# Performance work log

Measured on AMD Instinct MI355X. Metric: run time of the kernel, lower is better.

The kernel has to match this reference:

```python
import jax, jax.numpy as jnp
import numpy as np

H = 256; NH = 4; DH = H // NH
NT, NS, NV = 4096, 2048, 1024
E1, E2, E3 = 65536, 16384, 32768
LN_EPS = 1e-5


def setup_inputs() -> dict:
    key = jax.random.key(0)
    ks = jax.random.split(key, 40)
    def nrm(i, shape):
        return jax.random.normal(ks[i], shape, jnp.float32) * 0.05
    inp = {
        "x_term": jax.random.normal(ks[0], (NT, H), jnp.float32),
        "x_symbol": jax.random.normal(ks[1], (NS, H), jnp.float32),
        "x_var": jax.random.normal(ks[2], (NV, H), jnp.float32),
        "ha_src": jax.random.randint(ks[3], (E1,), 0, NT),
        "ha_dst": jax.random.randint(ks[4], (E1,), 0, NT),
        "so_src": jax.random.randint(ks[5], (E2,), 0, NT),
        "so_dst": jax.random.randint(ks[6], (E2,), 0, NS),
        "vo_src": jax.random.randint(ks[7], (E3,), 0, NV),
        "vo_dst": jax.random.randint(ks[8], (E3,), 0, NT),
        # SAGEConv params for the 4 term-destination relations
        "Wl_rha": nrm(9, (H, H)),  "bl_rha": nrm(10, (H,)), "Wr_rha": nrm(11, (H, H)),
        "Wl_ha":  nrm(12, (H, H)), "bl_ha":  nrm(13, (H,)), "Wr_ha":  nrm(14, (H, H)),
        "Wl_rsym": nrm(15, (H, H)), "bl_rsym": nrm(16, (H,)), "Wr_rsym": nrm(17, (H, H)),
        "Wl_var": nrm(18, (H, H)), "bl_var": nrm(19, (H,)), "Wr_var": nrm(20, (H, H)),
        "ln_g": jnp.ones((H,), jnp.float32),
        "ln_b": jnp.zeros((H,), jnp.float32),
        "in_proj_w": nrm(21, (3 * H, H)),
        "in_proj_b": nrm(22, (3 * H,)),
        "out_proj_w": nrm(23, (H, H)),
        "out_proj_b": nrm(24, (H,)),
        "post_w": nrm(25, (H, H)),
        "post_b": nrm(26, (H,)),
    }
    return inp


def _sage(x_src, x_dst, src, dst, Wl, bl, Wr, num_dst):
    # PyG SAGEConv: lin_l(mean_j x_src[j]) + lin_r(x_dst)
    msg = x_src[src]                                            # [E, H] gather
    s = jax.ops.segment_sum(msg, dst, num_segments=num_dst)     # [N_dst, H] scatter-add
    cnt = jax.ops.segment_sum(jnp.ones((src.shape[0],), x_src.dtype), dst,
                              num_segments=num_dst)
    agg = s / jnp.maximum(cnt, 1.0)[:, None]
    return agg @ Wl.T + bl + x_dst @ Wr.T


def _layernorm(x, g, b):
    mu = jnp.mean(x, axis=-1, keepdims=True)
    var = jnp.mean(jnp.square(x - mu), axis=-1, keepdims=True)
    return (x - mu) * jax.lax.rsqrt(var + LN_EPS) * g + b


def _mha(x, in_w, in_b, out_w, out_b):
    # torch MultiheadAttention (eval, batch=1, self-attention)
    qkv = x @ in_w.T + in_b                       # [N, 3H]
    q, k, v = jnp.split(qkv, 3, axis=-1)
    def heads(t):
        return t.reshape(-1, NH, DH).transpose(1, 0, 2)  # [NH, N, DH]
    q, k, v = heads(q), heads(k), heads(v)
    scores = jnp.einsum("hqd,hkd->hqk", q, k) / np.sqrt(DH).astype(np.float32)
    a = jax.nn.softmax(scores, axis=-1)
    o = jnp.einsum("hqk,hkd->hqd", a, v)          # [NH, N, DH]
    o = o.transpose(1, 0, 2).reshape(-1, H)
    return o @ out_w.T + out_b


def reference(x_term, x_symbol, x_var,
              ha_src, ha_dst, so_src, so_dst, vo_src, vo_dst,
              Wl_rha, bl_rha, Wr_rha, Wl_ha, bl_ha, Wr_ha,
              Wl_rsym, bl_rsym, Wr_rsym, Wl_var, bl_var, Wr_var,
              ln_g, ln_b, in_proj_w, in_proj_b, out_proj_w, out_proj_b,
              post_w, post_b):
    nt = x_term.shape[0]
    # HeteroConv(aggr='sum') over the 4 relations whose destination is 'term'
    conv_term = (
        _sage(x_term, x_term, ha_dst, ha_src, Wl_rha, bl_rha, Wr_rha, nt)    # rev_has_arg
        + _sage(x_term, x_term, ha_src, ha_dst, Wl_ha, bl_ha, Wr_ha, nt)     # has_arg
        + _sage(x_symbol, x_term, so_dst, so_src, Wl_rsym, bl_rsym, Wr_rsym, nt)  # rev_symbol_of
        + _sage(x_var, x_term, vo_src, vo_dst, Wl_var, bl_var, Wr_var, nt)   # var_occurrence
    )
    term_out = _layernorm(conv_term + x_term, ln_g, ln_b)  # dropout is identity in eval
    attn_out = _mha(term_out, in_proj_w, in_proj_b, out_proj_w, out_proj_b)
    post = jax.nn.relu(attn_out @ post_w.T + post_b)
    term_final = post + term_out
    return term_final
```

## Files before the change

kernel.cpp:

```cpp
#include <hip/hip_runtime.h>
#include <hip/hip_bf16.h>

#define H 256
#define NT 4096
#define NHEAD 4
#define E1 65536
#define E2 16384
#define E3 32768
#define TOTE (2 * E1 + E2 + E3)
#define LN_EPS 1e-5f
#define SPLIT 4

typedef __hip_bfloat16 bf16;
typedef short bf16x8 __attribute__((ext_vector_type(8)));
typedef float f32x4 __attribute__((ext_vector_type(4)));

__device__ __forceinline__ float b2f(bf16 v) { return __bfloat162float(v); }
__device__ __forceinline__ float u2f(unsigned short u) {
    unsigned int x = ((unsigned int)u) << 16;
    return __uint_as_float(x);
}
__device__ __forceinline__ unsigned short f2u(float f) {
    bf16 h = __float2bfloat16(f);
    unsigned short v;
    __builtin_memcpy(&v, &h, 2);
    return v;
}
__device__ __forceinline__ unsigned short f2u_rtz(float f) {
    return (unsigned short)(__float_as_uint(f) >> 16);
}
__device__ __forceinline__ float ldin(const void* p, size_t i, bool isbf) {
    return isbf ? b2f(((const bf16*)p)[i]) : ((const float*)p)[i];
}

__global__ __launch_bounds__(256) void k_init(float4* cnt4, int n4,
                                              const unsigned int* __restrict__ lng,
                                              unsigned int* __restrict__ flag) {
    int i = blockIdx.x * 256 + threadIdx.x;
    if (i == 0) *flag = (lng[0] == 0x3F803F80u) ? 1u : 0u;
    int stride = gridDim.x * 256;
    float4 z = make_float4(0.f, 0.f, 0.f, 0.f);
    for (; i < n4; i += stride) cnt4[i] = z;
}

__global__ __launch_bounds__(256) void k_count4(const int* __restrict__ s0, const int* __restrict__ s1,
                                                const int* __restrict__ s2, const int* __restrict__ s3,
                                                int* __restrict__ cnt) {
    int i = blockIdx.x * 256 + threadIdx.x;
    int r, e;
    if (i < E1) { r = 0; e = i; }
    else if (i < 2 * E1) { r = 1; e = i - E1; }
    else if (i < 2 * E1 + E2) { r = 2; e = i - 2 * E1; }
    else if (i < TOTE) { r = 3; e = i - 2 * E1 - E2; }
    else return;
    const int* s = (r == 0) ? s0 : (r == 1) ? s1 : (r == 2) ? s2 : s3;
    atomicAdd(&cnt[r * NT + s[e]], 1);
}

__global__ __launch_bounds__(256) void k_scan(const int* __restrict__ cnt, int* __restrict__ offs,
                                              int* __restrict__ cursor) {
    __shared__ int tot[256];
    int t = threadIdx.x, r = blockIdx.x;
    const int* c = cnt + r * NT;
    int* o = offs + r * (NT + 1);
    int* cur = cursor + r * NT;
    int base = t * 16;
    int local[16];
    int sum = 0;
#pragma unroll
    for (int j = 0; j < 16; j++) { local[j] = c[base + j]; sum += local[j]; }
    tot[t] = sum;
    __syncthreads();
    if (t == 0) {
        int run = 0;
        for (int i = 0; i < 256; i++) { int v = tot[i]; tot[i] = run; run += v; }
        o[NT] = run;
    }
    __syncthreads();
    int run = tot[t];
#pragma unroll
    for (int j = 0; j < 16; j++) { o[base + j] = run; cur[base + j] = run; run += local[j]; }
}

__global__ __launch_bounds__(256) void k_fill(const int* __restrict__ s0, const int* __restrict__ s1,
                                              const int* __restrict__ s2, const int* __restrict__ s3,
                                              const int* __restrict__ g0, const int* __restrict__ g1,
                                              const int* __restrict__ g2, const int* __restrict__ g3,
                                              int* __restrict__ cursor, int* __restrict__ csr) {
    int i = blockIdx.x * 256 + threadIdx.x;
    int r, e, rb;
    if (i < E1) { r = 0; e = i; rb = 0; }
    else if (i < 2 * E1) { r = 1; e = i - E1; rb = E1; }
    else if (i < 2 * E1 + E2) { r = 2; e = i - 2 * E1; rb = 2 * E1; }
    else if (i < TOTE) { r = 3; e = i - 2 * E1 - E2; rb = 2 * E1 + E2; }
    else return;
    const int* s = (r == 0) ? s0 : (r == 1) ? s1 : (r == 2) ? s2 : s3;
    const int* g = (r == 0) ? g0 : (r == 1) ? g1 : (r == 2) ? g2 : g3;
    int d = s[e];
    int pos = atomicAdd(&cursor[r * NT + d], 1);
    csr[rb + pos] = g[e];
}

__global__ __launch_bounds__(256) void k_gatherA(
    const void* __restrict__ x0, const void* __restrict__ x1,
    const void* __restrict__ x2, const void* __restrict__ x3,
    const int* __restrict__ offs, const int* __restrict__ csr,
    bf16* __restrict__ aggs, const unsigned int* __restrict__ flag) {
    int y = blockIdx.y;
    int i = blockIdx.x * 4 + (threadIdx.x >> 6);
    int lane = threadIdx.x & 63;
    bool isbf = (*flag != 0u);
    const void* x = (y == 0) ? x0 : (y == 1) ? x1 : (y == 2) ? x2 : x3;
    static const int rbase[4] = {0, E1, 2 * E1, 2 * E1 + E2};
    const int* o = offs + y * (NT + 1);
    const int* cs = csr + rbase[y];
    int b = o[i], e = o[i + 1];
    float ax = 0.f, ay = 0.f, az = 0.f, aw = 0.f;
    if (isbf) {
        for (int j = b; j < e; j++) {
            int s = cs[j];
            ushort4 u = *(const ushort4*)((const unsigned short*)x + (size_t)s * H + lane * 4);
            ax += u2f(u.x); ay += u2f(u.y); az += u2f(u.z); aw += u2f(u.w);
        }
    } else {
        for (int j = b; j < e; j++) {
            int s = cs[j];
            float4 v = *(const float4*)((const float*)x + (size_t)s * H + lane * 4);
            ax += v.x; ay += v.y; az += v.z; aw += v.w;
        }
    }
    float inv = 1.0f / fmaxf((float)(e - b), 1.0f);
    *(ushort4*)((unsigned short*)aggs + ((size_t)y * NT + i) * H + lane * 4) =
        make_ushort4(f2u(ax * inv), f2u(ay * inv), f2u(az * inv), f2u(aw * inv));
}

__global__ __launch_bounds__(256) void k_prepB(
    const void* __restrict__ Wl0, const void* __restrict__ Wl1,
    const void* __restrict__ Wl2, const void* __restrict__ Wl3,
    const void* __restrict__ Wr0, const void* __restrict__ Wr1,
    const void* __restrict__ Wr2, const void* __restrict__ Wr3,
    const void* __restrict__ b0, const void* __restrict__ b1,
    const void* __restrict__ b2, const void* __restrict__ b3,
    bf16* __restrict__ Bcat, float* __restrict__ bsum, const unsigned int* __restrict__ flag) {
    int idx = blockIdx.x * 256 + threadIdx.x;
    bool isbf = (*flag != 0u);
    int n = idx / 1280, k = idx % 1280;
    float v;
    if (k < 1024) {
        const void* W = (k < 256) ? Wl0 : (k < 512) ? Wl1 : (k < 768) ? Wl2 : Wl3;
        v = ldin(W, (size_t)n * 256 + (k & 255), isbf);
    } else {
        size_t o = (size_t)n * 256 + (k - 1024);
        v = ldin(Wr0, o, isbf) + ldin(Wr1, o, isbf) + ldin(Wr2, o, isbf) + ldin(Wr3, o, isbf);
    }
    ((unsigned short*)Bcat)[idx] = f2u(v);
    if (idx < 256)
        bsum[idx] = ldin(b0, idx, isbf) + ldin(b1, idx, isbf) + ldin(b2, idx, isbf) + ldin(b3, idx, isbf);
}

__global__ __launch_bounds__(256) void k_convln(
    const bf16* __restrict__ aggs, const bf16* __restrict__ Bcat, const float* __restrict__ bsum,
    const void* __restrict__ xt, const void* __restrict__ gw, const void* __restrict__ gb,
    bf16* __restrict__ term, const unsigned int* __restrict__ flag) {
    __shared__ unsigned short Asm[8 * 16 * 8];
    __shared__ unsigned short Bsm[8 * 256 * 8];
    __shared__ float redS[4][16];
    const bool isbf = (*flag != 0u);
    const int tid = threadIdx.x;
    const int w = tid >> 6, lane = tid & 63;
    const int col = lane & 15, quad = lane >> 4;
    const int m0 = blockIdx.x * 16;
    const int srow = tid & 63, skq = tid >> 6;

    f32x4 acc[4];
#pragma unroll
    for (int dt = 0; dt < 4; dt++) acc[dt] = (f32x4){0.f, 0.f, 0.f, 0.f};

    bf16x8 areg;
    bf16x8 breg[8];
    auto loadA = [&](int k0) {
        if (tid < 128) {
            int row = tid & 15, akq = tid >> 4;
            int k = k0 + akq * 8;
            if (k < 1024) {
                areg = *(const bf16x8*)((const unsigned short*)aggs +
                                        ((size_t)(k >> 8) * NT + m0 + row) * 256 + (k & 255));
            } else {
#pragma unroll
                for (int j = 0; j < 8; j++)
                    areg[j] = (short)f2u(ldin(xt, (size_t)(m0 + row) * 256 + (k - 1024) + j, isbf));
            }
        }
    };
    auto loadB = [&](int k0) {
#pragma unroll
        for (int t = 0; t < 4; t++)
#pragma unroll
            for (int kk = 0; kk < 2; kk++)
                breg[t * 2 + kk] = *(const bf16x8*)((const unsigned short*)Bcat +
                                       (size_t)(t * 64 + srow) * 1280 + k0 + (skq * 2 + kk) * 8);
    };

    loadA(0);
    loadB(0);
    for (int k0 = 0; k0 < 1280; k0 += 64) {
        __syncthreads();
        if (tid < 128) *(bf16x8*)&Asm[tid * 8] = areg;
#pragma unroll
        for (int t = 0; t < 4; t++)
#pragma unroll
            for (int kk = 0; kk < 2; kk++)
                *(bf16x8*)&Bsm[((skq * 2 + kk) * 256 + t * 64 + srow) * 8] = breg[t * 2 + kk];
        __syncthreads();
        if (k0 + 64 < 1280) { loadA(k0 + 64); loadB(k0 + 64); }
#pragma unroll
        for (int ch = 0; ch < 2; ch++) {
            bf16x8 a = *(const bf16x8*)&Asm[(((ch * 4 + quad) & 7) * 16 + col) * 8];
#pragma unroll
            for (int dt = 0; dt < 4; dt++) {
                bf16x8 b = *(const bf16x8*)&Bsm[((ch * 4 + quad) * 256 + w * 64 + dt * 16 + col) * 8];
                acc[dt] = __builtin_amdgcn_mfma_f32_16x16x32_bf16(a, b, acc[dt], 0, 0, 0);
            }
        }
    }

#pragma unroll
    for (int dt = 0; dt < 4; dt++) {
        int n = w * 64 + dt * 16 + col;
        float bsv = bsum[n];
#pragma unroll
        for (int r = 0; r < 4; r++) {
            int m = m0 + quad * 4 + r;
            acc[dt][r] += bsv + ldin(xt, (size_t)m * 256 + n, isbf);
        }
    }
    float mu[4], rs_[4];
#pragma unroll
    for (int r = 0; r < 4; r++) {
        float s = acc[0][r] + acc[1][r] + acc[2][r] + acc[3][r];
#pragma unroll
        for (int mk = 1; mk <= 8; mk <<= 1) s += __shfl_xor(s, mk);
        if (col == 0) redS[w][quad * 4 + r] = s;
    }
    __syncthreads();
#pragma unroll
    for (int r = 0; r < 4; r++) {
        int m = quad * 4 + r;
        mu[r] = (redS[0][m] + redS[1][m] + redS[2][m] + redS[3][m]) * (1.0f / 256.0f);
    }
    __syncthreads();
#pragma unroll
    for (int r = 0; r < 4; r++) {
        float s2 = 0.f;
#pragma unroll
        for (int dt = 0; dt < 4; dt++) {
            float d = acc[dt][r] - mu[r];
            s2 += d * d;
        }
#pragma unroll
        for (int mk = 1; mk <= 8; mk <<= 1) s2 += __shfl_xor(s2, mk);
        if (col == 0) redS[w][quad * 4 + r] = s2;
    }
    __syncthreads();
#pragma unroll
    for (int r = 0; r < 4; r++) {
        int m = quad * 4 + r;
        float var = (redS[0][m] + redS[1][m] + redS[2][m] + redS[3][m]) * (1.0f / 256.0f);
        rs_[r] = rsqrtf(var + LN_EPS);
    }
#pragma unroll
    for (int dt = 0; dt < 4; dt++) {
        int n = w * 64 + dt * 16 + col;
        float gv = ldin(gw, n, isbf), bv = ldin(gb, n, isbf);
#pragma unroll
        for (int r = 0; r < 4; r++) {
            int m = m0 + quad * 4 + r;
            term[(size_t)m * 256 + n] = __float2bfloat16((acc[dt][r] - mu[r]) * rs_[r] * gv + bv);
        }
    }
}

template <int AMODE, int EPI>
__global__ __launch_bounds__(256) void k_gemm(
    const void* __restrict__ A, const void* __restrict__ A2, const float* __restrict__ ml,
    const void* __restrict__ B, const void* __restrict__ bias,
    const bf16* __restrict__ resid, bf16* __restrict__ vt, void* __restrict__ outp,
    int M, int N, int K, const unsigned int* __restrict__ flag) {
    __shared__ unsigned short Asm[8 * 64 * 8];
    __shared__ unsigned short Bsm[8 * 64 * 8];
    const bool isbf = (*flag != 0u);
    const int tid = threadIdx.x;
    const int w = tid >> 6, lane = tid & 63;
    const int col = lane & 15, quad = lane >> 4;
    const int m0 = blockIdx.x * 64, n0 = blockIdx.y * 64;
    const int srow = tid & 63, skq = tid >> 6;
    const int am = m0 + srow;

    f32x4 acc[4];
#pragma unroll
    for (int dt = 0; dt < 4; dt++) acc[dt] = (f32x4){0.f, 0.f, 0.f, 0.f};

    bf16x8 areg[2], breg[2];
    auto loadA = [&](int k0) {
#pragma unroll
        for (int c = 0; c < 2; c++) {
            int k = k0 + skq * 16 + c * 8;
            if (AMODE == 0) {
                areg[c] = *(const bf16x8*)((const unsigned short*)A + (size_t)am * K + k);
            } else {
                int h = k >> 6;
                float l0 = ml[(size_t)(0 * NHEAD + h) * NT + am];
                float l1 = ml[(size_t)(1 * NHEAD + h) * NT + am];
                float l2 = ml[(size_t)(2 * NHEAD + h) * NT + am];
                float l3 = ml[(size_t)(3 * NHEAD + h) * NT + am];
                float iw = 1.0f / (l0 + l1 + l2 + l3);
                bf16x8 o0 = *(const bf16x8*)((const unsigned short*)A + (size_t)am * H + k);
                bf16x8 o1 = *(const bf16x8*)((const unsigned short*)A + ((size_t)NT + am) * H + k);
                bf16x8 o2 = *(const bf16x8*)((const unsigned short*)A2 + (size_t)am * H + k);
                bf16x8 o3 = *(const bf16x8*)((const unsigned short*)A2 + ((size_t)NT + am) * H + k);
#pragma unroll
                for (int j = 0; j < 8; j++)
                    areg[c][j] = (short)f2u((l0 * u2f((unsigned short)o0[j]) + l1 * u2f((unsigned short)o1[j]) +
                                             l2 * u2f((unsigned short)o2[j]) + l3 * u2f((unsigned short)o3[j])) * iw);
            }
        }
    };
    auto loadB = [&](int k0) {
#pragma unroll
        for (int c = 0; c < 2; c++) {
            size_t bi = (size_t)(n0 + srow) * K + k0 + skq * 16 + c * 8;
            if (isbf) {
                breg[c] = *(const bf16x8*)((const unsigned short*)B + bi);
            } else {
#pragma unroll
                for (int j = 0; j < 8; j++) breg[c][j] = (short)f2u(((const float*)B)[bi + j]);
            }
        }
    };

    loadA(0);
    loadB(0);
    for (int k0 = 0; k0 < K; k0 += 64) {
        __syncthreads();
#pragma unroll
        for (int c = 0; c < 2; c++) {
            *(bf16x8*)&Asm[((skq * 2 + c) * 64 + srow) * 8] = areg[c];
            *(bf16x8*)&Bsm[((skq * 2 + c) * 64 + srow) * 8] = breg[c];
        }
        __syncthreads();
        if (k0 + 64 < K) { loadA(k0 + 64); loadB(k0 + 64); }
#pragma unroll
        for (int ch = 0; ch < 2; ch++) {
            bf16x8 a = *(const bf16x8*)&Asm[((ch * 4 + quad) * 64 + w * 16 + col) * 8];
#pragma unroll
            for (int dt = 0; dt < 4; dt++) {
                bf16x8 b = *(const bf16x8*)&Bsm[((ch * 4 + quad) * 64 + dt * 16 + col) * 8];
                acc[dt] = __builtin_amdgcn_mfma_f32_16x16x32_bf16(a, b, acc[dt], 0, 0, 0);
            }
        }
    }
#pragma unroll
    for (int dt = 0; dt < 4; dt++) {
        int n = n0 + dt * 16 + col;
        float bv = ldin(bias, n, isbf);
        if (EPI == 3 && n0 >= 512) {
            int m = m0 + w * 16 + quad * 4;
            *(ushort4*)((unsigned short*)vt + (size_t)(n - 512) * NT + m) =
                make_ushort4(f2u(acc[dt][0] + bv), f2u(acc[dt][1] + bv),
                             f2u(acc[dt][2] + bv), f2u(acc[dt][3] + bv));
            continue;
        }
#pragma unroll
        for (int r = 0; r < 4; r++) {
            int m = m0 + w * 16 + quad * 4 + r;
            float v = acc[dt][r] + bv;
            if (EPI == 3) {
                ((bf16*)outp)[(size_t)m * 512 + n] = __float2bfloat16(v);
            } else if (EPI == 2) {
                size_t off = (size_t)m * N + n;
                v = fmaxf(v, 0.f);
                v += b2f(resid[off]);
                ((float*)outp)[off] = v;
            } else {
                ((bf16*)outp)[(size_t)m * N + n] = __float2bfloat16(v);
            }
        }
    }
}

__global__ __launch_bounds__(256) void k_attn(const bf16* __restrict__ qkvQK,
                                              const bf16* __restrict__ vt,
                                              bf16* __restrict__ opart01,
                                              bf16* __restrict__ opart23,
                                              float* __restrict__ ml) {
    __shared__ unsigned short Ksm[8 * 64 * 8];
    __shared__ unsigned short Vsm[8 * 64 * 8];
    __shared__ unsigned short Psm[4][2048];
    const int h = blockIdx.y, sp = blockIdx.z;
    const int q0 = blockIdx.x * 128;
    const int tid = threadIdx.x;
    const int w = tid >> 6, lane = tid & 63;
    const int col = lane & 15, quad = lane >> 4;
    const unsigned short* qk = (const unsigned short*)qkvQK;
    const unsigned short* vp = (const unsigned short*)vt;

    bf16x8 aQ[2][2];
#pragma unroll
    for (int qt = 0; qt < 2; qt++)
#pragma unroll
        for (int ch = 0; ch < 2; ch++)
            aQ[qt][ch] = *(const bf16x8*)(qk + (size_t)(q0 + qt * 64 + w * 16 + col) * 512 +
                                          h * 64 + ch * 32 + quad * 8);

    f32x4 O[2][4];
#pragma unroll
    for (int qt = 0; qt < 2; qt++)
#pragma unroll
        for (int dt = 0; dt < 4; dt++) O[qt][dt] = (f32x4){0.f, 0.f, 0.f, 0.f};
    float lsum[2] = {0.f, 0.f};

    const int kbeg = sp * (NT / SPLIT), kend = kbeg + NT / SPLIT;
    const float SC = 0.125f * 1.44269504f;
    const int pbase = col * 8 + (quad & 1) * 4 + (quad >> 1) * 128;

    bf16x8 kreg[2], vreg[2];
    auto loadKV = [&](int kb) {
#pragma unroll
        for (int it = 0; it < 2; it++) {
            int cid = tid + it * 256;
            int kkey = cid & 63, dhq = cid >> 6;
            kreg[it] = *(const bf16x8*)(qk + (size_t)(kb + kkey) * 512 + 256 + h * 64 + dhq * 8);
            int vd = cid & 63, vo = cid >> 6;
            vreg[it] = *(const bf16x8*)(vp + (size_t)(h * 64 + vd) * NT + kb + vo * 8);
        }
    };
    loadKV(kbeg);

    for (int kb = kbeg; kb < kend; kb += 64) {
        __syncthreads();
#pragma unroll
        for (int it = 0; it < 2; it++) {
            int cid = tid + it * 256;
            *(bf16x8*)&Ksm[cid * 8] = kreg[it];
            *(bf16x8*)&Vsm[cid * 8] = vreg[it];
        }
        __syncthreads();
        if (kb + 64 < kend) loadKV(kb + 64);

        f32x4 c0[4], c1[4];
#pragma unroll
        for (int dt = 0; dt < 4; dt++) {
            c0[dt] = (f32x4){0.f, 0.f, 0.f, 0.f};
            c1[dt] = (f32x4){0.f, 0.f, 0.f, 0.f};
#pragma unroll
            for (int ch = 0; ch < 2; ch++) {
                bf16x8 kf = *(const bf16x8*)&Ksm[((ch * 4 + quad) * 64 + dt * 16 + col) * 8];
                c0[dt] = __builtin_amdgcn_mfma_f32_16x16x32_bf16(kf, aQ[0][ch], c0[dt], 0, 0, 0);
                c1[dt] = __builtin_amdgcn_mfma_f32_16x16x32_bf16(kf, aQ[1][ch], c1[dt], 0, 0, 0);
            }
        }
#pragma unroll
        for (int qt = 0; qt < 2; qt++) {
#pragma unroll
            for (int dt = 0; dt < 4; dt++) {
                f32x4 cc = qt ? c1[dt] : c0[dt];
                float p0 = exp2f(cc[0] * SC), p1 = exp2f(cc[1] * SC);
                float p2 = exp2f(cc[2] * SC), p3 = exp2f(cc[3] * SC);
                lsum[qt] += (p0 + p1) + (p2 + p3);
                *(ushort4*)&Psm[w][qt * 1024 + dt * 256 + pbase] =
                    make_ushort4(f2u_rtz(p0), f2u_rtz(p1), f2u_rtz(p2), f2u_rtz(p3));
            }
        }
        bf16x8 aP[2][2];
#pragma unroll
        for (int qt = 0; qt < 2; qt++)
#pragma unroll
            for (int kc = 0; kc < 2; kc++)
                aP[qt][kc] = *(const bf16x8*)&Psm[w][qt * 1024 + (kc * 4 + quad) * 128 + col * 8];
#pragma unroll
        for (int dt = 0; dt < 4; dt++)
#pragma unroll
            for (int kc = 0; kc < 2; kc++) {
                bf16x8 b = *(const bf16x8*)&Vsm[((kc * 4 + quad) * 64 + dt * 16 + col) * 8];
                O[0][dt] = __builtin_amdgcn_mfma_f32_16x16x32_bf16(aP[0][kc], b, O[0][dt], 0, 0, 0);
                O[1][dt] = __builtin_amdgcn_mfma_f32_16x16x32_bf16(aP[1][kc], b, O[1][dt], 0, 0, 0);
            }
    }
#pragma unroll
    for (int qt = 0; qt < 2; qt++) {
        float l = lsum[qt];
        l += __shfl_xor(l, 16);
        l += __shfl_xor(l, 32);
        bf16* ob = (sp < 2) ? (opart01 + (size_t)sp * NT * H) : (opart23 + (size_t)(sp - 2) * NT * H);
        if (quad == 0)
            ml[((size_t)sp * NHEAD + h) * NT + (q0 + qt * 64 + w * 16 + col)] = l;
        float lr[4];
#pragma unroll
        for (int r = 0; r < 4; r++) lr[r] = __shfl(l, quad * 4 + r, 16);
#pragma unroll
        for (int dt = 0; dt < 4; dt++) {
#pragma unroll
            for (int r = 0; r < 4; r++) {
                int q = q0 + qt * 64 + w * 16 + quad * 4 + r;
                ob[(size_t)q * H + h * 64 + dt * 16 + col] = __float2bfloat16(O[qt][dt][r] / lr[r]);
            }
        }
    }
}

extern "C" void kernel_launch(void* const* d_in, const int* in_sizes, int n_in,
                              void* d_out, int out_size, void* d_ws, size_t ws_size,
                              hipStream_t stream) {
    const void* x_term   = d_in[0];
    const void* x_symbol = d_in[1];
    const void* x_var    = d_in[2];
    const int* ha_src = (const int*)d_in[3];
    const int* ha_dst = (const int*)d_in[4];
    const int* so_src = (const int*)d_in[5];
    const int* so_dst = (const int*)d_in[6];
    const int* vo_src = (const int*)d_in[7];
    const int* vo_dst = (const int*)d_in[8];
    const void* Wl[4]  = {d_in[9],  d_in[12], d_in[15], d_in[18]};
    const void* blv[4] = {d_in[10], d_in[13], d_in[16], d_in[19]};
    const void* Wr[4]  = {d_in[11], d_in[14], d_in[17], d_in[20]};
    const void* ln_g = d_in[21];
    const void* ln_b = d_in[22];
    const void* in_w = d_in[23];
    const void* in_b = d_in[24];
    const void* out_w = d_in[25];
    const void* out_b = d_in[26];
    const void* post_w = d_in[27];
    const void* post_b = d_in[28];

    char* ws = (char*)d_ws;
    unsigned int* flag = (unsigned int*)ws;
    char* csrbase = ws + 256;
    int* cnt    = (int*)csrbase;
    int* offs   = (int*)(csrbase + 65536);
    int* cursor = (int*)(csrbase + 132096);
    int* csr    = (int*)(csrbase + 197632);
    bf16*  Bcat = (bf16*)csrbase;
    float* bsum = (float*)(csrbase + 655360);
    float* ml   = (float*)csrbase;
    bf16* aggs  = (bf16*)(ws + (1 << 20));
    bf16* term  = (bf16*)(ws + (1 << 20) + 8388608);
    bf16* opart23 = (bf16*)(ws + (1 << 20) + 10485760);
    bf16* qkvQK = aggs;
    bf16* vt    = (bf16*)((char*)aggs + 4194304);
    bf16* proj  = aggs;
    bf16* opart01 = (bf16*)d_out;

    k_init<<<16, 256, 0, stream>>>((float4*)cnt, 4 * NT / 4, (const unsigned int*)ln_g, flag);
    k_count4<<<(TOTE + 255) / 256, 256, 0, stream>>>(ha_src, ha_dst, so_src, vo_dst, cnt);
    k_scan<<<4, 256, 0, stream>>>(cnt, offs, cursor);
    k_fill<<<(TOTE + 255) / 256, 256, 0, stream>>>(ha_src, ha_dst, so_src, vo_dst,
                                                   ha_dst, ha_src, so_dst, vo_src, cursor, csr);
    k_gatherA<<<dim3(NT / 4, 4), 256, 0, stream>>>(x_term, x_term, x_symbol, x_var,
                                                   offs, csr, aggs, flag);
    k_prepB<<<(256 * 1280) / 256, 256, 0, stream>>>(Wl[0], Wl[1], Wl[2], Wl[3],
                                                    Wr[0], Wr[1], Wr[2], Wr[3],
                                                    blv[0], blv[1], blv[2], blv[3],
                                                    Bcat, bsum, flag);

    k_convln<<<256, 256, 0, stream>>>(aggs, Bcat, bsum, x_term, ln_g, ln_b, term, flag);

    k_gemm<0, 3><<<dim3(64, 12), 256, 0, stream>>>(
        term, nullptr, nullptr, in_w, in_b, nullptr, vt, qkvQK, NT, 768, 256, flag);

    k_attn<<<dim3(32, NHEAD, SPLIT), 256, 0, stream>>>(qkvQK, vt, opart01, opart23, ml);

    k_gemm<1, 0><<<dim3(64, 4), 256, 0, stream>>>(
        opart01, opart23, ml, out_w, out_b, nullptr, nullptr, proj, NT, 256, 256, flag);

    k_gemm<0, 2><<<dim3(64, 4), 256, 0, stream>>>(
        proj, nullptr, nullptr, post_w, post_b, term, nullptr, d_out, NT, 256, 256, flag);

    (void)in_sizes; (void)n_in; (void)out_size; (void)ws_size;
}
```

Baseline: 276.9 us.

## Halve attention query tile to 64 rows, doubling blocks; add MFMA priority hints

The attention kernel now processes 64 queries per block instead of 128, doubling the grid to 1024 blocks and halving per-thread accumulator registers and the P buffer in LDS. This is meant to raise occupancy and parallelism on the many CUs. In exchange, each K/V tile loaded into shared memory is reused across half as many queries, doubling K/V global traffic. It also wraps the MFMA loops in s_setprio and switches to the hardware exp2 builtin.

```diff
diff --git a/kernel.cpp b/kernel.cpp
--- a/kernel.cpp
+++ b/kernel.cpp
@@ -395,29 +395,25 @@
                                               float* __restrict__ ml) {
     __shared__ unsigned short Ksm[8 * 64 * 8];
     __shared__ unsigned short Vsm[8 * 64 * 8];
-    __shared__ unsigned short Psm[4][2048];
+    __shared__ unsigned short Psm[4][1024];
     const int h = blockIdx.y, sp = blockIdx.z;
-    const int q0 = blockIdx.x * 128;
+    const int q0 = blockIdx.x * 64;
     const int tid = threadIdx.x;
     const int w = tid >> 6, lane = tid & 63;
     const int col = lane & 15, quad = lane >> 4;
     const unsigned short* qk = (const unsigned short*)qkvQK;
     const unsigned short* vp = (const unsigned short*)vt;
 
-    bf16x8 aQ[2][2];
-#pragma unroll
-    for (int qt = 0; qt < 2; qt++)
-#pragma unroll
-        for (int ch = 0; ch < 2; ch++)
-            aQ[qt][ch] = *(const bf16x8*)(qk + (size_t)(q0 + qt * 64 + w * 16 + col) * 512 +
-                                          h * 64 + ch * 32 + quad * 8);
-
-    f32x4 O[2][4];
-#pragma unroll
-    for (int qt = 0; qt < 2; qt++)
-#pragma unroll
-        for (int dt = 0; dt < 4; dt++) O[qt][dt] = (f32x4){0.f, 0.f, 0.f, 0.f};
-    float lsum[2] = {0.f, 0.f};
+    bf16x8 aQ[2];
+#pragma unroll
+    for (int ch = 0; ch < 2; ch++)
+        aQ[ch] = *(const bf16x8*)(qk + (size_t)(q0 + w * 16 + col) * 512 +
+                                  h * 64 + ch * 32 + quad * 8);
+
+    f32x4 O[4];
+#pragma unroll
+    for (int dt = 0; dt < 4; dt++) O[dt] = (f32x4){0.f, 0.f, 0.f, 0.f};
+    float lsum = 0.f;
 
     const int kbeg = sp * (NT / SPLIT), kend = kbeg + NT / SPLIT;
     const float SC = 0.125f * 1.44269504f;
@@ -447,63 +443,57 @@
         __syncthreads();
         if (kb + 64 < kend) loadKV(kb + 64);
 
-        f32x4 c0[4], c1[4];
+        f32x4 c[4];
+        __builtin_amdgcn_s_setprio(1);
 #pragma unroll
         for (int dt = 0; dt < 4; dt++) {
-            c0[dt] = (f32x4){0.f, 0.f, 0.f, 0.f};
-            c1[dt] = (f32x4){0.f, 0.f, 0.f, 0.f};
+            c[dt] = (f32x4){0.f, 0.f, 0.f, 0.f};
 #pragma unroll
             for (int ch = 0; ch < 2; ch++) {
                 bf16x8 kf = *(const bf16x8*)&Ksm[((ch * 4 + quad) * 64 + dt * 16 + col) * 8];
-                c0[dt] = __builtin_amdgcn_mfma_f32_16x16x32_bf16(kf, aQ[0][ch], c0[dt], 0, 0, 0);
-                c1[dt] = __builtin_amdgcn_mfma_f32_16x16x32_bf16(kf, aQ[1][ch], c1[dt], 0, 0, 0);
-            }
-        }
-#pragma unroll
-        for (int qt = 0; qt < 2; qt++) {
-#pragma unroll
-            for (int dt = 0; dt < 4; dt++) {
-                f32x4 cc = qt ? c1[dt] : c0[dt];
-                float p0 = exp2f(cc[0] * SC), p1 = exp2f(cc[1] * SC);
-                float p2 = exp2f(cc[2] * SC), p3 = exp2f(cc[3] * SC);
-                lsum[qt] += (p0 + p1) + (p2 + p3);
-                *(ushort4*)&Psm[w][qt * 1024 + dt * 256 + pbase] =
-                    make_ushort4(f2u_rtz(p0), f2u_rtz(p1), f2u_rtz(p2), f2u_rtz(p3));
-            }
-        }
-        bf16x8 aP[2][2];
-#pragma unroll
-        for (int qt = 0; qt < 2; qt++)
-#pragma unroll
-            for (int kc = 0; kc < 2; kc++)
-                aP[qt][kc] = *(const bf16x8*)&Psm[w][qt * 1024 + (kc * 4 + quad) * 128 + col * 8];
+                c[dt] = __builtin_amdgcn_mfma_f32_16x16x32_bf16(kf, aQ[ch], c[dt], 0, 0, 0);
+            }
+        }
+        __builtin_amdgcn_s_setprio(0);
+#pragma unroll
+        for (int dt = 0; dt < 4; dt++) {
+            float p0 = __builtin_amdgcn_exp2f(c[dt][0] * SC);
+            float p1 = __builtin_amdgcn_exp2f(c[dt][1] * SC);
+            float p2 = __builtin_amdgcn_exp2f(c[dt][2] * SC);
+            float p3 = __builtin_amdgcn_exp2f(c[dt][3] * SC);
+            lsum += (p0 + p1) + (p2 + p3);
+            *(ushort4*)&Psm[w][dt * 256 + pbase] =
+                make_ushort4(f2u_rtz(p0), f2u_rtz(p1), f2u_rtz(p2), f2u_rtz(p3));
+        }
+        bf16x8 aP[2];
+#pragma unroll
+        for (int kc = 0; kc < 2; kc++)
+            aP[kc] = *(const bf16x8*)&Psm[w][(kc * 4 + quad) * 128 + col * 8];
+        __builtin_amdgcn_s_setprio(1);
 #pragma unroll
         for (int dt = 0; dt < 4; dt++)
 #pragma unroll
             for (int kc = 0; kc < 2; kc++) {
                 bf16x8 b = *(const bf16x8*)&Vsm[((kc * 4 + quad) * 64 + dt * 16 + col) * 8];
-                O[0][dt] = __builtin_amdgcn_mfma_f32_16x16x32_bf16(aP[0][kc], b, O[0][dt], 0, 0, 0);
-                O[1][dt] = __builtin_amdgcn_mfma_f32_16x16x32_bf16(aP[1][kc], b, O[1][dt], 0, 0, 0);
-            }
-    }
-#pragma unroll
-    for (int qt = 0; qt < 2; qt++) {
-        float l = lsum[qt];
-        l += __shfl_xor(l, 16);
-        l += __shfl_xor(l, 32);
-        bf16* ob = (sp < 2) ? (opart01 + (size_t)sp * NT * H) : (opart23 + (size_t)(sp - 2) * NT * H);
-        if (quad == 0)
-            ml[((size_t)sp * NHEAD + h) * NT + (q0 + qt * 64 + w * 16 + col)] = l;
-        float lr[4];
-#pragma unroll
-        for (int r = 0; r < 4; r++) lr[r] = __shfl(l, quad * 4 + r, 16);
-#pragma unroll
-        for (int dt = 0; dt < 4; dt++) {
-#pragma unroll
-            for (int r = 0; r < 4; r++) {
-                int q = q0 + qt * 64 + w * 16 + quad * 4 + r;
-                ob[(size_t)q * H + h * 64 + dt * 16 + col] = __float2bfloat16(O[qt][dt][r] / lr[r]);
-            }
+                O[dt] = __builtin_amdgcn_mfma_f32_16x16x32_bf16(aP[kc], b, O[dt], 0, 0, 0);
+            }
+        __builtin_amdgcn_s_setprio(0);
+    }
+    float l = lsum;
+    l += __shfl_xor(l, 16);
+    l += __shfl_xor(l, 32);
+    bf16* ob = (sp < 2) ? (opart01 + (size_t)sp * NT * H) : (opart23 + (size_t)(sp - 2) * NT * H);
+    if (quad == 0)
+        ml[((size_t)sp * NHEAD + h) * NT + (q0 + w * 16 + col)] = l;
+    float lr[4];
+#pragma unroll
+    for (int r = 0; r < 4; r++) lr[r] = __shfl(l, quad * 4 + r, 16);
+#pragma unroll
+    for (int dt = 0; dt < 4; dt++) {
+#pragma unroll
+        for (int r = 0; r < 4; r++) {
+            int q = q0 + w * 16 + quad * 4 + r;
+            ob[(size_t)q * H + h * 64 + dt * 16 + col] = __float2bfloat16(O[dt][r] / lr[r]);
         }
     }
 }
@@ -567,7 +557,7 @@
     k_gemm<0, 3><<<dim3(64, 12), 256, 0, stream>>>(
         term, nullptr, nullptr, in_w, in_b, nullptr, vt, qkvQK, NT, 768, 256, flag);
 
-    k_attn<<<dim3(32, NHEAD, SPLIT), 256, 0, stream>>>(qkvQK, vt, opart01, opart23, ml);
+    k_attn<<<dim3(64, NHEAD, SPLIT), 256, 0, stream>>>(qkvQK, vt, opart01, opart23, ml);
 
     k_gemm<1, 0><<<dim3(64, 4), 256, 0, stream>>>(
         opart01, opart23, ml, out_w, out_b, nullptr, nullptr, proj, NT, 256, 256, flag);
```

New measurement: 275.0 us. No clear change (-0.7%).

## Load K/V MFMA fragments directly from global memory instead of LDS staging

Applied to the files above, without the earlier changes.

The attention kernel drops the shared-memory staging of K and V tiles. Each wave now loads its MFMA operand fragments straight from global memory (through L2/L1), which removes the two block-wide __syncthreads per key block and the LDS write/read traffic. In exchange it loses the register prefetch of the next tile and causes redundant global loads across the four waves. It also adds s_setprio around the MFMA sections, a bare s_barrier to keep waves in step, and uses the native exp2 builtin instead of exp2f.

```diff
diff --git a/kernel.cpp b/kernel.cpp
--- a/kernel.cpp
+++ b/kernel.cpp
@@ -393,8 +393,6 @@
                                               bf16* __restrict__ opart01,
                                               bf16* __restrict__ opart23,
                                               float* __restrict__ ml) {
-    __shared__ unsigned short Ksm[8 * 64 * 8];
-    __shared__ unsigned short Vsm[8 * 64 * 8];
     __shared__ unsigned short Psm[4][2048];
     const int h = blockIdx.y, sp = blockIdx.z;
     const int q0 = blockIdx.x * 128;
@@ -423,49 +421,46 @@
     const float SC = 0.125f * 1.44269504f;
     const int pbase = col * 8 + (quad & 1) * 4 + (quad >> 1) * 128;
 
-    bf16x8 kreg[2], vreg[2];
-    auto loadKV = [&](int kb) {
-#pragma unroll
-        for (int it = 0; it < 2; it++) {
-            int cid = tid + it * 256;
-            int kkey = cid & 63, dhq = cid >> 6;
-            kreg[it] = *(const bf16x8*)(qk + (size_t)(kb + kkey) * 512 + 256 + h * 64 + dhq * 8);
-            int vd = cid & 63, vo = cid >> 6;
-            vreg[it] = *(const bf16x8*)(vp + (size_t)(h * 64 + vd) * NT + kb + vo * 8);
-        }
-    };
-    loadKV(kbeg);
+    const unsigned short* kfb = qk + 256 + h * 64 + (size_t)col * 512 + quad * 8;
+    const unsigned short* vfb = vp + ((size_t)(h * 64 + col)) * NT + quad * 8;
 
     for (int kb = kbeg; kb < kend; kb += 64) {
-        __syncthreads();
-#pragma unroll
-        for (int it = 0; it < 2; it++) {
-            int cid = tid + it * 256;
-            *(bf16x8*)&Ksm[cid * 8] = kreg[it];
-            *(bf16x8*)&Vsm[cid * 8] = vreg[it];
-        }
-        __syncthreads();
-        if (kb + 64 < kend) loadKV(kb + 64);
+        bf16x8 kf[2][4];
+#pragma unroll
+        for (int dt = 0; dt < 4; dt++)
+#pragma unroll
+            for (int ch = 0; ch < 2; ch++)
+                kf[ch][dt] = *(const bf16x8*)(kfb + (size_t)(kb + dt * 16) * 512 + ch * 32);
+        bf16x8 vf[2][4];
+#pragma unroll
+        for (int dt = 0; dt < 4; dt++)
+#pragma unroll
+            for (int kc = 0; kc < 2; kc++)
+                vf[kc][dt] = *(const bf16x8*)(vfb + (size_t)(dt * 16) * NT + kb + kc * 32);
+        __builtin_amdgcn_s_barrier();
 
         f32x4 c0[4], c1[4];
+        __builtin_amdgcn_s_setprio(1);
 #pragma unroll
         for (int dt = 0; dt < 4; dt++) {
             c0[dt] = (f32x4){0.f, 0.f, 0.f, 0.f};
             c1[dt] = (f32x4){0.f, 0.f, 0.f, 0.f};
 #pragma unroll
             for (int ch = 0; ch < 2; ch++) {
-                bf16x8 kf = *(const bf16x8*)&Ksm[((ch * 4 + quad) * 64 + dt * 16 + col) * 8];
-                c0[dt] = __builtin_amdgcn_mfma_f32_16x16x32_bf16(kf, aQ[0][ch], c0[dt], 0, 0, 0);
-                c1[dt] = __builtin_amdgcn_mfma_f32_16x16x32_bf16(kf, aQ[1][ch], c1[dt], 0, 0, 0);
-            }
-        }
+                c0[dt] = __builtin_amdgcn_mfma_f32_16x16x32_bf16(kf[ch][dt], aQ[0][ch], c0[dt], 0, 0, 0);
+                c1[dt] = __builtin_amdgcn_mfma_f32_16x16x32_bf16(kf[ch][dt], aQ[1][ch], c1[dt], 0, 0, 0);
+            }
+        }
+        __builtin_amdgcn_s_setprio(0);
 #pragma unroll
         for (int qt = 0; qt < 2; qt++) {
 #pragma unroll
             for (int dt = 0; dt < 4; dt++) {
                 f32x4 cc = qt ? c1[dt] : c0[dt];
-                float p0 = exp2f(cc[0] * SC), p1 = exp2f(cc[1] * SC);
-                float p2 = exp2f(cc[2] * SC), p3 = exp2f(cc[3] * SC);
+                float p0 = __builtin_amdgcn_exp2f(cc[0] * SC);
+                float p1 = __builtin_amdgcn_exp2f(cc[1] * SC);
+                float p2 = __builtin_amdgcn_exp2f(cc[2] * SC);
+                float p3 = __builtin_amdgcn_exp2f(cc[3] * SC);
                 lsum[qt] += (p0 + p1) + (p2 + p3);
                 *(ushort4*)&Psm[w][qt * 1024 + dt * 256 + pbase] =
                     make_ushort4(f2u_rtz(p0), f2u_rtz(p1), f2u_rtz(p2), f2u_rtz(p3));
@@ -477,14 +472,15 @@
 #pragma unroll
             for (int kc = 0; kc < 2; kc++)
                 aP[qt][kc] = *(const bf16x8*)&Psm[w][qt * 1024 + (kc * 4 + quad) * 128 + col * 8];
+        __builtin_amdgcn_s_setprio(1);
 #pragma unroll
         for (int dt = 0; dt < 4; dt++)
 #pragma unroll
             for (int kc = 0; kc < 2; kc++) {
-                bf16x8 b = *(const bf16x8*)&Vsm[((kc * 4 + quad) * 64 + dt * 16 + col) * 8];
-                O[0][dt] = __builtin_amdgcn_mfma_f32_16x16x32_bf16(aP[0][kc], b, O[0][dt], 0, 0, 0);
-                O[1][dt] = __builtin_amdgcn_mfma_f32_16x16x32_bf16(aP[1][kc], b, O[1][dt], 0, 0, 0);
-            }
+                O[0][dt] = __builtin_amdgcn_mfma_f32_16x16x32_bf16(aP[0][kc], vf[kc][dt], O[0][dt], 0, 0, 0);
+                O[1][dt] = __builtin_amdgcn_mfma_f32_16x16x32_bf16(aP[1][kc], vf[kc][dt], O[1][dt], 0, 0, 0);
+            }
+        __builtin_amdgcn_s_setprio(0);
     }
 #pragma unroll
     for (int qt = 0; qt < 2; qt++) {
```

New measurement: 298.8 us. +7.9%, slower.
